# Kernel optimization log

Hardware: AMD Instinct MI355X
Metric: run time of the kernel (lower is better)

## Reference

```python
import jax, jax.numpy as jnp
import numpy as np

E = 128          # embedding_dimension
H = 8            # attention heads
HS = E // H      # head size = 16
HID = 512 * E    # FFN hidden = 65536 (output_scale=512 hardcoded)
B, T = 2, 2048
EPS = 1e-5


def setup_inputs() -> dict:
    key = jax.random.key(0)
    ks = jax.random.split(key, 12)
    s_e = 1.0 / np.sqrt(E)
    s_h = 1.0 / np.sqrt(HID)
    return {
        "x":   jax.random.normal(ks[0], (B, T, E), jnp.float32),
        # per-head K/Q/V projections, stacked: [H, E, HS] (Linear, no bias)
        "Wk":  jax.random.normal(ks[1], (H, E, HS), jnp.float32) * s_e,
        "Wq":  jax.random.normal(ks[2], (H, E, HS), jnp.float32) * s_e,
        "Wv":  jax.random.normal(ks[3], (H, E, HS), jnp.float32) * s_e,
        # output projection [E, E] + bias
        "Wo":  jax.random.normal(ks[4], (E, E), jnp.float32) * s_e,
        "bo":  jnp.zeros((E,), jnp.float32),
        # LayerNorms
        "g1":  jnp.ones((E,), jnp.float32),
        "be1": jnp.zeros((E,), jnp.float32),
        "g2":  jnp.ones((E,), jnp.float32),
        "be2": jnp.zeros((E,), jnp.float32),
        # FFN: E -> 512E -> E
        "W1":  jax.random.normal(ks[5], (E, HID), jnp.float32) * s_e,
        "bf1": jnp.zeros((HID,), jnp.float32),
        "W2":  jax.random.normal(ks[6], (HID, E), jnp.float32) * s_h,
        "bf2": jnp.zeros((E,), jnp.float32),
    }


def _layernorm(x, g, b):
    mu = jnp.mean(x, axis=-1, keepdims=True)
    var = jnp.mean(jnp.square(x - mu), axis=-1, keepdims=True)
    return (x - mu) * jax.lax.rsqrt(var + EPS) * g + b


def _block(x, Wk, Wq, Wv, Wo, bo, g1, be1, g2, be2, W1, bf1, W2, bf2):
    Bb, Tt, C = x.shape
    # --- multi-head causal self-attention (pre-LN) ---
    h = _layernorm(x, g1, be1)
    q = jnp.einsum("bte,hed->bhtd", h, Wq)
    k = jnp.einsum("bte,hed->bhtd", h, Wk)
    v = jnp.einsum("bte,hed->bhtd", h, Wv)
    # NOTE: original scales by C**-0.5 with C = embedding_dimension
    scores = jnp.einsum("bhtd,bhsd->bhts", q, k) * (C ** -0.5)
    causal = jnp.tril(jnp.ones((Tt, Tt), bool))
    scores = jnp.where(causal, scores, -jnp.inf)
    w = jax.nn.softmax(scores, axis=-1)           # [B,H,T,T]
    o = jnp.einsum("bhts,bhsd->bhtd", w, v)       # [B,H,T,HS]
    o = o.transpose(0, 2, 1, 3).reshape(Bb, Tt, C)  # concat heads
    sa = o @ Wo + bo
    x = x + sa
    # --- FFN (pre-LN) ---
    h2 = _layernorm(x, g2, be2)
    ff = jax.nn.relu(h2 @ W1 + bf1) @ W2 + bf2
    return x + ff


def reference(x, Wk, Wq, Wv, Wo, bo, g1, be1, g2, be2, W1, bf1, W2, bf2):
    return _block(x, Wk, Wq, Wv, Wo, bo, g1, be1, g2, be2, W1, bf1, W2, bf2)
```

## Files before the change

kernel.cpp:

```cpp
#include <hip/hip_runtime.h>

typedef __bf16 bf16x8 __attribute__((ext_vector_type(8)));
typedef float f32x16 __attribute__((ext_vector_type(16)));

#define DEV static __device__ __forceinline__
#define MFMA(a, b, c) __builtin_amdgcn_mfma_f32_32x32x16_bf16((a), (b), (c), 0, 0, 0)

DEV unsigned short f2bf(float f) {
  unsigned u = __float_as_uint(f);
  unsigned r = u + 0x7fffu + ((u >> 16) & 1u);
  return (unsigned short)(r >> 16);
}
DEV float bflo(unsigned u) { return __uint_as_float(u << 16); }
DEV float bfhi(unsigned u) { return __uint_as_float(u & 0xffff0000u); }

DEV f32x16 zero16() {
  f32x16 z;
#pragma unroll
  for (int i = 0; i < 16; i++) z[i] = 0.f;
  return z;
}

DEV bf16x8 frag256(const unsigned short* lds, int rowbase, int l, int kk) {
  int row = rowbase + (l & 31);
  int gran = (kk << 1) + (l >> 5);
  return *reinterpret_cast<const bf16x8*>(&lds[row * 128 + ((gran ^ (row & 7)) << 3)]);
}
DEV bf16x8 frag128(const unsigned short* lds, int rowbase, int l, int kk) {
  int row = rowbase + (l & 31);
  int gran = (kk << 1) + (l >> 5);
  return *reinterpret_cast<const bf16x8*>(&lds[row * 64 + ((gran ^ (row & 7)) << 3)]);
}

__global__ void k_transpose(const float* __restrict__ in, unsigned short* __restrict__ out,
                            int R, int C) {
  __shared__ float t[32][33];
  int tx = threadIdx.x, ty = threadIdx.y;
  int c0 = blockIdx.x * 32, r0 = blockIdx.y * 32;
#pragma unroll
  for (int i = 0; i < 4; i++)
    t[ty + i * 8][tx] = in[(size_t)(r0 + ty + i * 8) * C + c0 + tx];
  __syncthreads();
#pragma unroll
  for (int i = 0; i < 4; i++)
    out[(size_t)(c0 + ty + i * 8) * R + r0 + tx] = f2bf(t[tx][ty + i * 8]);
}

__global__ void k_build_qkvo(const float* __restrict__ Wq, const float* __restrict__ Wk,
                             const float* __restrict__ Wv, const float* __restrict__ Wo,
                             unsigned short* __restrict__ qkvt, unsigned short* __restrict__ wot) {
  int gid = blockIdx.x * 256 + threadIdx.x;
  if (gid < 49152) {
    int row = gid >> 7, e = gid & 127;
    int mi = row >> 7, c = row & 127, h = c >> 4, d = c & 15;
    const float* W = (mi == 0) ? Wq : (mi == 1) ? Wk : Wv;
    qkvt[gid] = f2bf(W[(h * 128 + e) * 16 + d]);
  } else {
    int id = gid - 49152;
    int n = id >> 7, k = id & 127;
    wot[id] = f2bf(Wo[k * 128 + n]);
  }
}

__global__ void k_ln(const float* __restrict__ x, const float* __restrict__ g,
                     const float* __restrict__ b, unsigned short* __restrict__ out) {
  int row = blockIdx.x * 4 + (threadIdx.x >> 6);
  int l = threadIdx.x & 63;
  const float* xr = x + (size_t)row * 128;
  float x0 = xr[l * 2], x1v = xr[l * 2 + 1];
  float s = x0 + x1v;
#pragma unroll
  for (int m = 1; m < 64; m <<= 1) s += __shfl_xor(s, m, 64);
  float mu = s * 0.0078125f;
  float d0 = x0 - mu, d1 = x1v - mu;
  float ss = d0 * d0 + d1 * d1;
#pragma unroll
  for (int m = 1; m < 64; m <<= 1) ss += __shfl_xor(ss, m, 64);
  float inv = rsqrtf(ss * 0.0078125f + 1e-5f);
  float y0 = d0 * inv * g[l * 2] + b[l * 2];
  float y1 = d1 * inv * g[l * 2 + 1] + b[l * 2 + 1];
  unsigned u = ((unsigned)f2bf(y1) << 16) | (unsigned)f2bf(y0);
  *reinterpret_cast<unsigned*>(out + (size_t)row * 128 + l * 2) = u;
}

__global__ void k_gemm_qkv(const unsigned short* __restrict__ A, const unsigned short* __restrict__ Bt,
                           unsigned short* __restrict__ qkv) {
  __shared__ __align__(16) unsigned short As[128 * 128];
  __shared__ __align__(16) unsigned short Bs[128 * 128];
  int tid = threadIdx.x;
  int m0 = blockIdx.x * 128, n0 = blockIdx.y * 128;
  int sg = tid & 15, sr = tid >> 4;
#pragma unroll
  for (int i = 0; i < 8; i++) {
    int r = sr + i * 16;
    *reinterpret_cast<bf16x8*>(&As[r * 128 + ((sg ^ (r & 7)) << 3)]) =
        *reinterpret_cast<const bf16x8*>(A + (size_t)(m0 + r) * 128 + sg * 8);
    *reinterpret_cast<bf16x8*>(&Bs[r * 128 + ((sg ^ (r & 7)) << 3)]) =
        *reinterpret_cast<const bf16x8*>(Bt + (size_t)(n0 + r) * 128 + sg * 8);
  }
  __syncthreads();
  int l = tid & 63, w = tid >> 6, wmi = w >> 1, wni = w & 1;
  int ln = l & 31, hi = l >> 5;
  f32x16 acc[2][2];
  acc[0][0] = zero16(); acc[0][1] = zero16(); acc[1][0] = zero16(); acc[1][1] = zero16();
#pragma unroll
  for (int kk = 0; kk < 8; kk++) {
    bf16x8 a0 = frag256(As, wmi * 64, l, kk);
    bf16x8 a1 = frag256(As, wmi * 64 + 32, l, kk);
    bf16x8 b0 = frag256(Bs, wni * 64, l, kk);
    bf16x8 b1 = frag256(Bs, wni * 64 + 32, l, kk);
    acc[0][0] = MFMA(a0, b0, acc[0][0]);
    acc[0][1] = MFMA(a0, b1, acc[0][1]);
    acc[1][0] = MFMA(a1, b0, acc[1][0]);
    acc[1][1] = MFMA(a1, b1, acc[1][1]);
  }
  unsigned short* mat = qkv + (size_t)blockIdx.y * 524288;
#pragma unroll
  for (int im = 0; im < 2; im++)
#pragma unroll
    for (int in_ = 0; in_ < 2; in_++) {
      int c = wni * 64 + in_ * 32 + ln;
      int h = c >> 4, d = c & 15;
#pragma unroll
      for (int r = 0; r < 16; r++) {
        int m = m0 + wmi * 64 + im * 32 + (r & 3) + ((r >> 2) << 3) + (hi << 2);
        int bb = m >> 11, tt = m & 2047;
        mat[((size_t)((bb << 3) + h) * 2048 + tt) * 16 + d] = f2bf(acc[im][in_][r]);
      }
    }
}

DEV bf16x8 pfrag(float a0, float a1, float a2, float a3,
                 float a4, float a5, float a6, float a7) {
  unsigned c0, c1, c2, c3;
  asm("v_cvt_pk_bf16_f32 %0, %1, %2" : "=v"(c0) : "v"(a0), "v"(a1));
  asm("v_cvt_pk_bf16_f32 %0, %1, %2" : "=v"(c1) : "v"(a2), "v"(a3));
  asm("v_cvt_pk_bf16_f32 %0, %1, %2" : "=v"(c2) : "v"(a4), "v"(a5));
  asm("v_cvt_pk_bf16_f32 %0, %1, %2" : "=v"(c3) : "v"(a6), "v"(a7));
  asm("v_permlane32_swap_b32 %0, %1" : "+v"(c0), "+v"(c2));
  asm("v_permlane32_swap_b32 %0, %1" : "+v"(c1), "+v"(c3));
  int4 ri = make_int4((int)c0, (int)c1, (int)c2, (int)c3);
  return *reinterpret_cast<bf16x8*>(&ri);
}

__global__ void __launch_bounds__(256)
k_attn2(const unsigned short* __restrict__ qw, const unsigned short* __restrict__ kw,
        const unsigned short* __restrict__ vw, unsigned short* __restrict__ ow) {
  __shared__ __align__(16) unsigned short vt[2][16][72];
  int tid = threadIdx.x;
  int qb = (int)gridDim.x - 1 - (int)blockIdx.x;
  int bh = blockIdx.y;
  int w = tid >> 6, l = tid & 63, ln = l & 31, hi = l >> 5;
  int q0 = qb * 128 + w * 32;
  int q = q0 + ln;
  const float SC = 0.08838834764831845f * 1.4426950408889634f;
  const unsigned short* kbase = kw + (size_t)bh * 32768;
  const unsigned short* vbase = vw + (size_t)bh * 32768;
  bf16x8 qf = *reinterpret_cast<const bf16x8*>(qw + (size_t)bh * 32768 + (size_t)q * 16 + hi * 8);
  f32x16 acc = zero16();
  float mr = -1e30f, ls = 0.f;
  int ntiles = 2 * qb + 2;
  int skey = tid >> 1, sh = tid & 1;
  for (int st = 0; st < ntiles; st++) {
    int k0 = st * 64;
    int buf = st & 1;
    if (tid < 128) {
      const unsigned* vp = reinterpret_cast<const unsigned*>(vbase + (size_t)(k0 + skey) * 16 + sh * 8);
      unsigned u0 = vp[0], u1 = vp[1], u2 = vp[2], u3 = vp[3];
      int d0 = sh * 8;
      vt[buf][d0 + 0][skey] = (unsigned short)u0;
      vt[buf][d0 + 1][skey] = (unsigned short)(u0 >> 16);
      vt[buf][d0 + 2][skey] = (unsigned short)u1;
      vt[buf][d0 + 3][skey] = (unsigned short)(u1 >> 16);
      vt[buf][d0 + 4][skey] = (unsigned short)u2;
      vt[buf][d0 + 5][skey] = (unsigned short)(u2 >> 16);
      vt[buf][d0 + 6][skey] = (unsigned short)u3;
      vt[buf][d0 + 7][skey] = (unsigned short)(u3 >> 16);
    }
    __syncthreads();
    if (k0 > q0 + 31) continue;
    bool d1 = (k0 + 32 <= q0 + 31);
    f32x16 p0, p1;
    {
      bf16x8 ka = *reinterpret_cast<const bf16x8*>(kbase + (size_t)(k0 + ln) * 16 + hi * 8);
      p0 = MFMA(ka, qf, zero16());
    }
    if (d1) {
      bf16x8 kb = *reinterpret_cast<const bf16x8*>(kbase + (size_t)(k0 + 32 + ln) * 16 + hi * 8);
      p1 = MFMA(kb, qf, zero16());
    }
    if (k0 + 31 > q0) {
#pragma unroll
      for (int r = 0; r < 16; r++) {
        int krow = (r & 3) + 8 * (r >> 2) + 4 * hi;
        if (k0 + krow > q) p0[r] = -1e30f;
      }
    }
    if (d1 && (k0 + 63 > q0)) {
#pragma unroll
      for (int r = 0; r < 16; r++) {
        int krow = (r & 3) + 8 * (r >> 2) + 4 * hi;
        if (k0 + 32 + krow > q) p1[r] = -1e30f;
      }
    }
    float tm = p0[0];
#pragma unroll
    for (int r = 1; r < 16; r++) tm = fmaxf(tm, p0[r]);
    if (d1) {
#pragma unroll
      for (int r = 0; r < 16; r++) tm = fmaxf(tm, p1[r]);
    }
    tm = fmaxf(tm, __shfl_xor(tm, 32, 64));
    if (tm > mr) {
      float corr = exp2f((mr - tm) * SC);
      ls *= corr;
#pragma unroll
      for (int r = 0; r < 8; r++) acc[r] *= corr;
      mr = tm;
    }
    float msc = mr * SC;
#pragma unroll
    for (int r = 0; r < 16; r++) {
      p0[r] = exp2f(fmaf(p0[r], SC, -msc));
      ls += p0[r];
    }
    if (d1) {
#pragma unroll
      for (int r = 0; r < 16; r++) {
        p1[r] = exp2f(fmaf(p1[r], SC, -msc));
        ls += p1[r];
      }
    }
    const unsigned short* vrow = &vt[buf][ln & 15][0];
    {
      bf16x8 pa = pfrag(p0[0], p0[1], p0[2], p0[3], p0[4], p0[5], p0[6], p0[7]);
      bf16x8 va = *reinterpret_cast<const bf16x8*>(vrow + hi * 8);
      acc = MFMA(va, pa, acc);
      pa = pfrag(p0[8], p0[9], p0[10], p0[11], p0[12], p0[13], p0[14], p0[15]);
      va = *reinterpret_cast<const bf16x8*>(vrow + 16 + hi * 8);
      acc = MFMA(va, pa, acc);
    }
    if (d1) {
      bf16x8 pa = pfrag(p1[0], p1[1], p1[2], p1[3], p1[4], p1[5], p1[6], p1[7]);
      bf16x8 va = *reinterpret_cast<const bf16x8*>(vrow + 32 + hi * 8);
      acc = MFMA(va, pa, acc);
      pa = pfrag(p1[8], p1[9], p1[10], p1[11], p1[12], p1[13], p1[14], p1[15]);
      va = *reinterpret_cast<const bf16x8*>(vrow + 48 + hi * 8);
      acc = MFMA(va, pa, acc);
    }
  }
  ls += __shfl_xor(ls, 32, 64);
  float rl = 1.0f / ls;
  int b_ = bh >> 3, h_ = bh & 7;
  unsigned short* op = ow + ((size_t)(b_ * 2048 + q)) * 128 + h_ * 16;
  int dbase = 4 * hi;
  unsigned o0 = ((unsigned)f2bf(acc[1] * rl) << 16) | (unsigned)f2bf(acc[0] * rl);
  unsigned o1 = ((unsigned)f2bf(acc[3] * rl) << 16) | (unsigned)f2bf(acc[2] * rl);
  unsigned o2 = ((unsigned)f2bf(acc[5] * rl) << 16) | (unsigned)f2bf(acc[4] * rl);
  unsigned o3 = ((unsigned)f2bf(acc[7] * rl) << 16) | (unsigned)f2bf(acc[6] * rl);
  *reinterpret_cast<unsigned*>(op + dbase) = o0;
  *reinterpret_cast<unsigned*>(op + dbase + 2) = o1;
  *reinterpret_cast<unsigned*>(op + 8 + dbase) = o2;
  *reinterpret_cast<unsigned*>(op + 8 + dbase + 2) = o3;
}

__global__ void k_gemm_proj(const unsigned short* __restrict__ A, const unsigned short* __restrict__ Bt,
                            const float* __restrict__ bo, const float* __restrict__ x,
                            const float* __restrict__ bf2, float* __restrict__ x1,
                            float* __restrict__ outp) {
  __shared__ __align__(16) unsigned short As[128 * 128];
  __shared__ __align__(16) unsigned short Bs[128 * 128];
  int tid = threadIdx.x;
  int m0 = blockIdx.x * 128;
  int sg = tid & 15, sr = tid >> 4;
#pragma unroll
  for (int i = 0; i < 8; i++) {
    int r = sr + i * 16;
    *reinterpret_cast<bf16x8*>(&As[r * 128 + ((sg ^ (r & 7)) << 3)]) =
        *reinterpret_cast<const bf16x8*>(A + (size_t)(m0 + r) * 128 + sg * 8);
    *reinterpret_cast<bf16x8*>(&Bs[r * 128 + ((sg ^ (r & 7)) << 3)]) =
        *reinterpret_cast<const bf16x8*>(Bt + (size_t)r * 128 + sg * 8);
  }
  __syncthreads();
  int l = tid & 63, w = tid >> 6, wmi = w >> 1, wni = w & 1;
  int ln = l & 31, hi = l >> 5;
  f32x16 acc[2][2];
  acc[0][0] = zero16(); acc[0][1] = zero16(); acc[1][0] = zero16(); acc[1][1] = zero16();
#pragma unroll
  for (int kk = 0; kk < 8; kk++) {
    bf16x8 a0 = frag256(As, wmi * 64, l, kk);
    bf16x8 a1 = frag256(As, wmi * 64 + 32, l, kk);
    bf16x8 b0 = frag256(Bs, wni * 64, l, kk);
    bf16x8 b1 = frag256(Bs, wni * 64 + 32, l, kk);
    acc[0][0] = MFMA(a0, b0, acc[0][0]);
    acc[0][1] = MFMA(a0, b1, acc[0][1]);
    acc[1][0] = MFMA(a1, b0, acc[1][0]);
    acc[1][1] = MFMA(a1, b1, acc[1][1]);
  }
#pragma unroll
  for (int im = 0; im < 2; im++)
#pragma unroll
    for (int in_ = 0; in_ < 2; in_++) {
      int n = wni * 64 + in_ * 32 + ln;
      float bon = bo[n], b2n = bf2[n];
#pragma unroll
      for (int r = 0; r < 16; r++) {
        int m = m0 + wmi * 64 + im * 32 + (r & 3) + ((r >> 2) << 3) + (hi << 2);
        float v = acc[im][in_][r] + bon;
        float xv = x[(size_t)m * 128 + n] + v;
        x1[(size_t)m * 128 + n] = xv;
        outp[(size_t)m * 128 + n] = xv + b2n;
      }
    }
}

__global__ void __launch_bounds__(256, 2)
k_ffn(const unsigned short* __restrict__ h2, const unsigned short* __restrict__ w1t,
      const unsigned short* __restrict__ w2t, const float* __restrict__ bf1,
      float* __restrict__ outp) {
  __shared__ __align__(16) unsigned short w1_lds[64 * 128];
  __shared__ __align__(16) unsigned short w2_lds[128 * 64];
  __shared__ __align__(16) unsigned short g_lds[128 * 64];
  int tid = threadIdx.x, l = tid & 63, w = tid >> 6;
  int wmi = w >> 1, wni = w & 1;
  int ln = l & 31, hi = l >> 5;
  int chunk = blockIdx.x & 15, rowblk = blockIdx.x >> 4;

  bf16x8 af[2][8];
#pragma unroll
  for (int im = 0; im < 2; im++) {
    int row = rowblk * 128 + wmi * 64 + im * 32 + ln;
#pragma unroll
    for (int kk = 0; kk < 8; kk++)
      af[im][kk] = *reinterpret_cast<const bf16x8*>(h2 + (size_t)row * 128 + kk * 16 + hi * 8);
  }

  f32x16 acc2[2][2];
  acc2[0][0] = zero16(); acc2[0][1] = zero16(); acc2[1][0] = zero16(); acc2[1][1] = zero16();

  int sg1 = tid & 15, sr1 = tid >> 4;
  int sg2 = tid & 7, sr2 = tid >> 3;

  for (int it = 0; it < 64; it++) {
    int hid0 = chunk * 4096 + it * 64;
#pragma unroll
    for (int i = 0; i < 4; i++) {
      int r = sr1 + i * 16;
      *reinterpret_cast<bf16x8*>(&w1_lds[r * 128 + ((sg1 ^ (r & 7)) << 3)]) =
          *reinterpret_cast<const bf16x8*>(w1t + (size_t)(hid0 + r) * 128 + sg1 * 8);
    }
#pragma unroll
    for (int i = 0; i < 4; i++) {
      int r = sr2 + i * 32;
      *reinterpret_cast<bf16x8*>(&w2_lds[r * 64 + ((sg2 ^ (r & 7)) << 3)]) =
          *reinterpret_cast<const bf16x8*>(w2t + (size_t)r * 65536 + hid0 + sg2 * 8);
    }
    __syncthreads();

    f32x16 acc1[2];
    acc1[0] = zero16(); acc1[1] = zero16();
#pragma unroll
    for (int kk = 0; kk < 8; kk++) {
      bf16x8 b = frag256(w1_lds, wni * 32, l, kk);
      acc1[0] = MFMA(af[0][kk], b, acc1[0]);
      acc1[1] = MFMA(af[1][kk], b, acc1[1]);
    }
    float b1v = bf1[hid0 + wni * 32 + ln];
    int gn = wni * 32 + ln;
    int ggr = gn >> 3, gof = gn & 7;
#pragma unroll
    for (int im = 0; im < 2; im++) {
#pragma unroll
      for (int r = 0; r < 16; r++) {
        int m = wmi * 64 + im * 32 + (r & 3) + ((r >> 2) << 3) + (hi << 2);
        float v = acc1[im][r] + b1v;
        v = v > 0.f ? v : 0.f;
        g_lds[m * 64 + ((ggr ^ (m & 7)) << 3) + gof] = f2bf(v);
      }
    }
    __syncthreads();

#pragma unroll
    for (int kk = 0; kk < 4; kk++) {
      bf16x8 a0 = frag128(g_lds, wmi * 64, l, kk);
      bf16x8 a1 = frag128(g_lds, wmi * 64 + 32, l, kk);
      bf16x8 b0 = frag128(w2_lds, wni * 64, l, kk);
      bf16x8 b1 = frag128(w2_lds, wni * 64 + 32, l, kk);
      acc2[0][0] = MFMA(a0, b0, acc2[0][0]);
      acc2[0][1] = MFMA(a0, b1, acc2[0][1]);
      acc2[1][0] = MFMA(a1, b0, acc2[1][0]);
      acc2[1][1] = MFMA(a1, b1, acc2[1][1]);
    }
    __syncthreads();
  }

#pragma unroll
  for (int im = 0; im < 2; im++)
#pragma unroll
    for (int in_ = 0; in_ < 2; in_++) {
      int n = wni * 64 + in_ * 32 + ln;
#pragma unroll
      for (int r = 0; r < 16; r++) {
        int m = rowblk * 128 + wmi * 64 + im * 32 + (r & 3) + ((r >> 2) << 3) + (hi << 2);
        atomicAdd(&outp[(size_t)m * 128 + n], acc2[im][in_][r]);
      }
    }
}

extern "C" void kernel_launch(void* const* d_in, const int* in_sizes, int n_in,
                              void* d_out, int out_size, void* d_ws, size_t ws_size,
                              hipStream_t stream) {
  (void)in_sizes; (void)n_in; (void)out_size; (void)ws_size;
  const float* x = (const float*)d_in[0];
  const float* Wk = (const float*)d_in[1];
  const float* Wq = (const float*)d_in[2];
  const float* Wv = (const float*)d_in[3];
  const float* Wo = (const float*)d_in[4];
  const float* bo = (const float*)d_in[5];
  const float* g1 = (const float*)d_in[6];
  const float* be1 = (const float*)d_in[7];
  const float* g2 = (const float*)d_in[8];
  const float* be2 = (const float*)d_in[9];
  const float* W1 = (const float*)d_in[10];
  const float* bf1 = (const float*)d_in[11];
  const float* W2 = (const float*)d_in[12];
  const float* bf2 = (const float*)d_in[13];
  float* outp = (float*)d_out;

  unsigned short* ws = (unsigned short*)d_ws;
  unsigned short* W1t = ws;
  unsigned short* W2t = ws + 8388608;
  unsigned short* Wqkvt = ws + 16777216;
  unsigned short* Wot = ws + 16826368;
  unsigned short* h1 = ws + 16842752;
  unsigned short* h2 = ws + 17367040;
  unsigned short* qw = ws + 17891328;
  unsigned short* kw = ws + 18415616;
  unsigned short* vw = ws + 18939904;
  unsigned short* ow = ws + 19464192;
  float* x1 = (float*)(ws + 19988480);

  k_transpose<<<dim3(2048, 4), dim3(32, 8), 0, stream>>>(W1, W1t, 128, 65536);
  k_transpose<<<dim3(4, 2048), dim3(32, 8), 0, stream>>>(W2, W2t, 65536, 128);
  k_build_qkvo<<<256, 256, 0, stream>>>(Wq, Wk, Wv, Wo, Wqkvt, Wot);
  k_ln<<<1024, 256, 0, stream>>>(x, g1, be1, h1);
  k_gemm_qkv<<<dim3(32, 3), 256, 0, stream>>>(h1, Wqkvt, qw);
  k_attn2<<<dim3(16, 16), 256, 0, stream>>>(qw, kw, vw, ow);
  k_gemm_proj<<<32, 256, 0, stream>>>(ow, Wot, bo, x, bf2, x1, outp);
  k_ln<<<1024, 256, 0, stream>>>(x1, g2, be2, h2);
  k_ffn<<<512, 256, 0, stream>>>(h2, W1t, W2t, bf1, outp);
}
```

Before: 394.2 us.

## Restructure fused FFN kernel with register-resident hidden activations and double-buffered weights

Replaces the FFN kernel with a version where each wave owns 64 rows and computes the transposed hidden tile (W1 times h) so the ReLU output can be packed straight into MFMA B-fragments in registers, with no LDS round trip for the intermediate. Weight tiles are prefetched into registers and written to a double-buffered LDS in fragment-native layout, leaving one barrier per iteration instead of three. Blocks now cover 256 rows, so the grid drops to 256 blocks with one block per CU by launch bounds. This raises register pressure and lowers occupancy in exchange for fewer syncs and less LDS traffic.

```diff
diff --git a/kernel.cpp b/kernel.cpp
--- a/kernel.cpp
+++ b/kernel.cpp
@@ -25,11 +25,6 @@
   int row = rowbase + (l & 31);
   int gran = (kk << 1) + (l >> 5);
   return *reinterpret_cast<const bf16x8*>(&lds[row * 128 + ((gran ^ (row & 7)) << 3)]);
-}
-DEV bf16x8 frag128(const unsigned short* lds, int rowbase, int l, int kk) {
-  int row = rowbase + (l & 31);
-  int gran = (kk << 1) + (l >> 5);
-  return *reinterpret_cast<const bf16x8*>(&lds[row * 64 + ((gran ^ (row & 7)) << 3)]);
 }
 
 __global__ void k_transpose(const float* __restrict__ in, unsigned short* __restrict__ out,
@@ -314,97 +309,114 @@
     }
 }
 
-__global__ void __launch_bounds__(256, 2)
-k_ffn(const unsigned short* __restrict__ h2, const unsigned short* __restrict__ w1t,
-      const unsigned short* __restrict__ w2t, const float* __restrict__ bf1,
-      float* __restrict__ outp) {
-  __shared__ __align__(16) unsigned short w1_lds[64 * 128];
-  __shared__ __align__(16) unsigned short w2_lds[128 * 64];
-  __shared__ __align__(16) unsigned short g_lds[128 * 64];
-  int tid = threadIdx.x, l = tid & 63, w = tid >> 6;
-  int wmi = w >> 1, wni = w & 1;
-  int ln = l & 31, hi = l >> 5;
-  int chunk = blockIdx.x & 15, rowblk = blockIdx.x >> 4;
-
-  bf16x8 af[2][8];
-#pragma unroll
-  for (int im = 0; im < 2; im++) {
-    int row = rowblk * 128 + wmi * 64 + im * 32 + ln;
+__global__ void __launch_bounds__(256, 1)
+k_ffn2(const unsigned short* __restrict__ h2, const unsigned short* __restrict__ w1t,
+       const unsigned short* __restrict__ w2t, const float* __restrict__ bf1,
+       float* __restrict__ outp) {
+  __shared__ __align__(16) unsigned short lA[2][16][512];
+  __shared__ __align__(16) unsigned short lB[2][16][512];
+  int tid = threadIdx.x, w = tid >> 6, l = tid & 63, ln = l & 31, hi = l >> 5;
+  int chunk = blockIdx.x & 15, mblk = blockIdx.x >> 4;
+  int m0 = mblk * 256 + w * 64;
+
+  bf16x8 hb[2][8];
+#pragma unroll
+  for (int mh = 0; mh < 2; mh++)
 #pragma unroll
     for (int kk = 0; kk < 8; kk++)
-      af[im][kk] = *reinterpret_cast<const bf16x8*>(h2 + (size_t)row * 128 + kk * 16 + hi * 8);
-  }
-
-  f32x16 acc2[2][2];
-  acc2[0][0] = zero16(); acc2[0][1] = zero16(); acc2[1][0] = zero16(); acc2[1][1] = zero16();
-
-  int sg1 = tid & 15, sr1 = tid >> 4;
-  int sg2 = tid & 7, sr2 = tid >> 3;
-
-  for (int it = 0; it < 64; it++) {
-    int hid0 = chunk * 4096 + it * 64;
-#pragma unroll
-    for (int i = 0; i < 4; i++) {
-      int r = sr1 + i * 16;
-      *reinterpret_cast<bf16x8*>(&w1_lds[r * 128 + ((sg1 ^ (r & 7)) << 3)]) =
-          *reinterpret_cast<const bf16x8*>(w1t + (size_t)(hid0 + r) * 128 + sg1 * 8);
-    }
-#pragma unroll
-    for (int i = 0; i < 4; i++) {
-      int r = sr2 + i * 32;
-      *reinterpret_cast<bf16x8*>(&w2_lds[r * 64 + ((sg2 ^ (r & 7)) << 3)]) =
-          *reinterpret_cast<const bf16x8*>(w2t + (size_t)r * 65536 + hid0 + sg2 * 8);
+      hb[mh][kk] = *reinterpret_cast<const bf16x8*>(
+          h2 + (size_t)(m0 + mh * 32 + ln) * 128 + kk * 16 + hi * 8);
+
+  f32x16 acc[4][2];
+#pragma unroll
+  for (int et = 0; et < 4; et++) { acc[et][0] = zero16(); acc[et][1] = zero16(); }
+
+  uint4 stA[4], stB[4];
+  {
+    int nn = chunk * 4096;
+#pragma unroll
+    for (int p = 0; p < 4; p++) {
+      int F = p * 4 + w;
+      stA[p] = *reinterpret_cast<const uint4*>(
+          w1t + (size_t)(nn + (F >> 3) * 32 + ln) * 128 + (F & 7) * 16 + hi * 8);
+      stB[p] = *reinterpret_cast<const uint4*>(
+          w2t + (size_t)((F >> 2) * 32 + ln) * 65536 + nn + (F & 3) * 16 + hi * 8);
+    }
+#pragma unroll
+    for (int p = 0; p < 4; p++) {
+      int F = p * 4 + w;
+      *reinterpret_cast<uint4*>(&lA[0][F][l * 8]) = stA[p];
+      *reinterpret_cast<uint4*>(&lB[0][F][l * 8]) = stB[p];
+    }
+  }
+  __syncthreads();
+
+  int cur = 0;
+  for (int t = 0; t < 64; t++) {
+    if (t < 63) {
+      int nn = chunk * 4096 + (t + 1) * 64;
+#pragma unroll
+      for (int p = 0; p < 4; p++) {
+        int F = p * 4 + w;
+        stA[p] = *reinterpret_cast<const uint4*>(
+            w1t + (size_t)(nn + (F >> 3) * 32 + ln) * 128 + (F & 7) * 16 + hi * 8);
+        stB[p] = *reinterpret_cast<const uint4*>(
+            w2t + (size_t)((F >> 2) * 32 + ln) * 65536 + nn + (F & 3) * 16 + hi * 8);
+      }
+    }
+    int n0 = chunk * 4096 + t * 64;
+    const unsigned short* A = &lA[cur][0][0];
+    const unsigned short* B = &lB[cur][0][0];
+#pragma unroll
+    for (int sub = 0; sub < 2; sub++) {
+      f32x16 g0 = zero16(), g1 = zero16();
+#pragma unroll
+      for (int kk = 0; kk < 8; kk++) {
+        bf16x8 a = *reinterpret_cast<const bf16x8*>(A + (sub * 8 + kk) * 512 + l * 8);
+        g0 = MFMA(a, hb[0][kk], g0);
+        g1 = MFMA(a, hb[1][kk], g1);
+      }
+#pragma unroll
+      for (int r = 0; r < 16; r++) {
+        float bv = bf1[n0 + sub * 32 + (r & 3) + 8 * (r >> 2) + 4 * hi];
+        g0[r] = fmaxf(g0[r] + bv, 0.f);
+        g1[r] = fmaxf(g1[r] + bv, 0.f);
+      }
+      bf16x8 pb00 = pfrag(g0[0], g0[1], g0[2], g0[3], g0[4], g0[5], g0[6], g0[7]);
+      bf16x8 pb01 = pfrag(g0[8], g0[9], g0[10], g0[11], g0[12], g0[13], g0[14], g0[15]);
+      bf16x8 pb10 = pfrag(g1[0], g1[1], g1[2], g1[3], g1[4], g1[5], g1[6], g1[7]);
+      bf16x8 pb11 = pfrag(g1[8], g1[9], g1[10], g1[11], g1[12], g1[13], g1[14], g1[15]);
+#pragma unroll
+      for (int et = 0; et < 4; et++) {
+        bf16x8 wa0 = *reinterpret_cast<const bf16x8*>(B + (et * 4 + sub * 2 + 0) * 512 + l * 8);
+        acc[et][0] = MFMA(wa0, pb00, acc[et][0]);
+        acc[et][1] = MFMA(wa0, pb10, acc[et][1]);
+        bf16x8 wa1 = *reinterpret_cast<const bf16x8*>(B + (et * 4 + sub * 2 + 1) * 512 + l * 8);
+        acc[et][0] = MFMA(wa1, pb01, acc[et][0]);
+        acc[et][1] = MFMA(wa1, pb11, acc[et][1]);
+      }
+    }
+    if (t < 63) {
+#pragma unroll
+      for (int p = 0; p < 4; p++) {
+        int F = p * 4 + w;
+        *reinterpret_cast<uint4*>(&lA[cur ^ 1][F][l * 8]) = stA[p];
+        *reinterpret_cast<uint4*>(&lB[cur ^ 1][F][l * 8]) = stB[p];
+      }
     }
     __syncthreads();
-
-    f32x16 acc1[2];
-    acc1[0] = zero16(); acc1[1] = zero16();
-#pragma unroll
-    for (int kk = 0; kk < 8; kk++) {
-      bf16x8 b = frag256(w1_lds, wni * 32, l, kk);
-      acc1[0] = MFMA(af[0][kk], b, acc1[0]);
-      acc1[1] = MFMA(af[1][kk], b, acc1[1]);
-    }
-    float b1v = bf1[hid0 + wni * 32 + ln];
-    int gn = wni * 32 + ln;
-    int ggr = gn >> 3, gof = gn & 7;
-#pragma unroll
-    for (int im = 0; im < 2; im++) {
-#pragma unroll
-      for (int r = 0; r < 16; r++) {
-        int m = wmi * 64 + im * 32 + (r & 3) + ((r >> 2) << 3) + (hi << 2);
-        float v = acc1[im][r] + b1v;
-        v = v > 0.f ? v : 0.f;
-        g_lds[m * 64 + ((ggr ^ (m & 7)) << 3) + gof] = f2bf(v);
-      }
-    }
-    __syncthreads();
-
-#pragma unroll
-    for (int kk = 0; kk < 4; kk++) {
-      bf16x8 a0 = frag128(g_lds, wmi * 64, l, kk);
-      bf16x8 a1 = frag128(g_lds, wmi * 64 + 32, l, kk);
-      bf16x8 b0 = frag128(w2_lds, wni * 64, l, kk);
-      bf16x8 b1 = frag128(w2_lds, wni * 64 + 32, l, kk);
-      acc2[0][0] = MFMA(a0, b0, acc2[0][0]);
-      acc2[0][1] = MFMA(a0, b1, acc2[0][1]);
-      acc2[1][0] = MFMA(a1, b0, acc2[1][0]);
-      acc2[1][1] = MFMA(a1, b1, acc2[1][1]);
-    }
-    __syncthreads();
-  }
-
-#pragma unroll
-  for (int im = 0; im < 2; im++)
-#pragma unroll
-    for (int in_ = 0; in_ < 2; in_++) {
-      int n = wni * 64 + in_ * 32 + ln;
-#pragma unroll
-      for (int r = 0; r < 16; r++) {
-        int m = rowblk * 128 + wmi * 64 + im * 32 + (r & 3) + ((r >> 2) << 3) + (hi << 2);
-        atomicAdd(&outp[(size_t)m * 128 + n], acc2[im][in_][r]);
-      }
-    }
+    cur ^= 1;
+  }
+#pragma unroll
+  for (int et = 0; et < 4; et++)
+#pragma unroll
+    for (int mh = 0; mh < 2; mh++)
+#pragma unroll
+      for (int r = 0; r < 16; r++) {
+        int e = et * 32 + (r & 3) + 8 * (r >> 2) + 4 * hi;
+        int m = m0 + mh * 32 + ln;
+        atomicAdd(&outp[(size_t)m * 128 + e], acc[et][mh][r]);
+      }
 }
 
 extern "C" void kernel_launch(void* const* d_in, const int* in_sizes, int n_in,
@@ -448,5 +460,5 @@
   k_attn2<<<dim3(16, 16), 256, 0, stream>>>(qw, kw, vw, ow);
   k_gemm_proj<<<32, 256, 0, stream>>>(ow, Wot, bo, x, bf2, x1, outp);
   k_ln<<<1024, 256, 0, stream>>>(x1, g2, be2, h2);
-  k_ffn<<<512, 256, 0, stream>>>(h2, W1t, W2t, bf1, outp);
-}
+  k_ffn2<<<256, 256, 0, stream>>>(h2, W1t, W2t, bf1, outp);
+}
```

New measurement: 749.0 us. 1.9x slower.
